# Performance work log

Hardware: AMD Instinct MI355X
Metric: run time of the kernel (lower is better)

Reference implementation:

```python
import jax, jax.numpy as jnp
import numpy as np

# Explicit-duration HSMM forward DP in log space.
# Recursion (all quantities in log space):
#   entry[t, j] = pi[j]                                   if t == 0
#               = logsumexp_i alpha[t-1, i] + A[i, j]      otherwise
#   alpha[t, j] = logsumexp_{d=1..min(Dmax, t+1)}
#                   entry[t-d+1, j] + D[j, d] + sum_{u=t-d+1..t} log_B[u, j]
#   loglik      = logsumexp_j alpha[T-1, j]

NEG = -1.0e30  # finite -inf sentinel (autodiff-safe)
B, T, S, DMAX = 64, 2048, 128, 128


def setup_inputs() -> dict:
    key = jax.random.key(0)
    k1, k2, k3, k4 = jax.random.split(key, 4)
    # emission log-likelihoods per (batch, time, state); need not normalize over states
    log_B = jax.random.normal(k1, (B, T, S), dtype=jnp.float32)
    # normalized log-prob buffers, matching the module's buffer constraints
    pi_logits = jax.nn.log_softmax(jax.random.normal(k2, (S,), dtype=jnp.float32))
    A_raw = jax.random.normal(k3, (S, S), dtype=jnp.float32)
    # SEMI transition constraint: no self-transitions (diagonal ~ -inf), rows normalized
    A_logits = jax.nn.log_softmax(
        jnp.where(jnp.eye(S, dtype=bool), -1.0e9, A_raw), axis=1)
    D_logits = jax.nn.log_softmax(
        jax.random.normal(k4, (S, DMAX), dtype=jnp.float32), axis=1)
    return {"log_B": log_B, "pi_logits": pi_logits,
            "A_logits": A_logits, "D_logits": D_logits}


def _hsmm_forward_loglik(log_B, pi_logits, A_logits, D_logits):
    Bn, Tn, Sn = log_B.shape
    Dm = D_logits.shape[1]
    lb = jnp.transpose(log_B, (1, 0, 2))                         # (T, B, S)
    # cum[k] = sum_{u < k} log_B[u]; front-padded with Dm zero rows (masked anyway)
    cum = jnp.concatenate(
        [jnp.zeros((1, Bn, Sn), lb.dtype), jnp.cumsum(lb, axis=0)], axis=0)
    cum_pad = jnp.concatenate(
        [jnp.zeros((Dm, Bn, Sn), lb.dtype), cum], axis=0)        # (T+Dm+1, B, S)
    logD = D_logits.T[:, None, :]                                # (Dm, 1, S)
    dur = jnp.arange(1, Dm + 1)[:, None, None]                   # (Dm, 1, 1)

    def step(carry, t):
        entry_buf, alpha_prev = carry                            # (Dm,B,S), (B,S)
        # transition into state j after a segment ended at t-1
        trans = jax.nn.logsumexp(
            alpha_prev[:, :, None] + A_logits[None, :, :], axis=1)  # (B, S)
        entry_t = jnp.where(t == 0, pi_logits[None, :], trans)
        # entry_buf[d-1] = entry[t-d+1]
        entry_buf = jnp.roll(entry_buf, 1, axis=0).at[0].set(entry_t)
        # segment emission sums: seg[d-1] = cum[t+1] - cum[t+1-d]
        win = jax.lax.dynamic_slice_in_dim(cum_pad, t + 1, Dm, axis=0)
        end = jax.lax.dynamic_slice_in_dim(cum_pad, t + Dm + 1, 1, axis=0)
        seg = end - jnp.flip(win, axis=0)                        # (Dm, B, S)
        scores = entry_buf + logD + seg
        scores = jnp.where(dur <= t + 1, scores, NEG)            # mask d > t+1
        alpha_t = jax.nn.logsumexp(scores, axis=0)               # (B, S)
        return (entry_buf, alpha_t), None

    init = (jnp.full((Dm, Bn, Sn), NEG, lb.dtype),
            jnp.full((Bn, Sn), NEG, lb.dtype))
    (_, alpha_last), _ = jax.lax.scan(step, init, jnp.arange(Tn))
    return jax.nn.logsumexp(alpha_last, axis=1)                  # (B,)


def reference(log_B, pi_logits, A_logits, D_logits):
    return _hsmm_forward_loglik(log_B, pi_logits, A_logits, D_logits)
```

## Files before the change

### kernel.cpp

```cpp
#include <hip/hip_runtime.h>

#define TT 2048
#define SS 128
#define DMAXX 128
#define NBATCH 64

typedef float f2 __attribute__((ext_vector_type(2)));

__device__ __forceinline__ float fexp2(float x){ return __builtin_amdgcn_exp2f(x); }
__device__ __forceinline__ float flog2(float x){ return __builtin_amdgcn_logf(x); }
__device__ __forceinline__ float frcp (float x){ return __builtin_amdgcn_rcpf(x); }
__device__ __forceinline__ f2 pkfma(f2 a, f2 b, f2 c){ return __builtin_elementwise_fma(a, b, c); }

template<int CTRL>
__device__ __forceinline__ float dppf(float x) {
    int i = __float_as_int(x);
    return __int_as_float(__builtin_amdgcn_update_dpp(i, i, CTRL, 0xF, 0xF, false));
}
#define DPP_XOR1   0xB1
#define DPP_XOR2   0x4E
#define DPP_SHUP1  0x90
#define DPP_ROR4   0x124
#define DPP_ROR8   0x128
#define DPP_BC15   0x142
#define DPP_BC31   0x143

constexpr float LOG2E = 1.4426950408889634f;
constexpr float LN2   = 0.6931471805599453f;

struct State {
    f2    rp[16];
    f2    eAp[16];
    f2    eDp[32];
    float eD0;
    float pf[4];
    const float* pfp;
    float C2;
    float e_pi;
};

struct Ctx {
    const float4* up0; const float4* up1;
    const f2*     wmp;
    float* uaw0; float* uaw1;
    float* wmwp;
    bool q0, l63;
};

template<int PHI>
__device__ __forceinline__ void hsmm_step(State& st, const Ctx& c, int tb)
{
    constexpr int  rho   = 31 - PHI;
    constexpr int  pb    = (PHI + 1) & 1;
    constexpr int  wb    = PHI & 1;
    constexpr bool DO_WM = ((PHI & 7) == 6);
    constexpr bool DO_RN = ((PHI & 7) == 7);
    const int t = tb + PHI;

    const float4* up = pb ? c.up1 : c.up0;
    float4 v[8];
#pragma unroll
    for (int k = 0; k < 8; ++k) v[k] = up[k];

    float xB = st.pf[PHI & 3];
    if (t + 4 < TT) st.pf[PHI & 3] = st.pfp[0];
    st.pfp += SS;
    float g = fexp2(xB * LOG2E);
    if constexpr (DO_RN) {
        f2 wv = *c.wmp;
        float m = fmaxf(wv.x, wv.y);
        m = fmaxf(m, dppf<DPP_XOR1>(m));
        m = fmaxf(m, dppf<DPP_XOR2>(m));
        st.C2 += flog2(m);
        g *= frcp(m);
    }

    float rold;
    if constexpr (rho & 1) rold = st.rp[rho >> 1].y; else rold = st.rp[rho >> 1].x;
    float car  = dppf<DPP_SHUP1>(rold);
    float insg = (c.q0 ? 0.f : car) * g;
    f2 gg = {g, g};
#pragma unroll
    for (int m2 = 0; m2 < 16; ++m2) st.rp[m2] = st.rp[m2] * gg;
    if constexpr (rho & 1) st.rp[rho >> 1].y = insg;
    else                   st.rp[rho >> 1].x = insg;

    f2 q0a = {0.f, 0.f}, q1a = {0.f, 0.f}, q2a = {0.f, 0.f}, q3a = {0.f, 0.f};
#pragma unroll
    for (int m2 = 0; m2 < 16; m2 += 4) {
        q0a = pkfma(st.rp[m2],     st.eDp[(2 * m2 + PHI + 1) & 31], q0a);
        q1a = pkfma(st.rp[m2 + 1], st.eDp[(2 * m2 + PHI + 3) & 31], q1a);
        q2a = pkfma(st.rp[m2 + 2], st.eDp[(2 * m2 + PHI + 5) & 31], q2a);
        q3a = pkfma(st.rp[m2 + 3], st.eDp[(2 * m2 + PHI + 7) & 31], q3a);
    }
    f2 qs = (q0a + q1a) + (q2a + q3a);
    float ds = qs.x + qs.y;
    ds += dppf<DPP_XOR1>(ds);
    ds += dppf<DPP_XOR2>(ds);

    f2 a0, a1, a2, a3;
    {
        f2 u;
        u = (f2){v[0].x, v[0].y}; a0 = u * st.eAp[0];
        u = (f2){v[0].z, v[0].w}; a1 = u * st.eAp[1];
        u = (f2){v[1].x, v[1].y}; a2 = u * st.eAp[2];
        u = (f2){v[1].z, v[1].w}; a3 = u * st.eAp[3];
#pragma unroll
        for (int kk = 2; kk < 8; kk += 2) {
            u = (f2){v[kk].x,     v[kk].y};     a0 = pkfma(u, st.eAp[2 * kk],     a0);
            u = (f2){v[kk].z,     v[kk].w};     a1 = pkfma(u, st.eAp[2 * kk + 1], a1);
            u = (f2){v[kk + 1].x, v[kk + 1].y}; a2 = pkfma(u, st.eAp[2 * kk + 2], a2);
            u = (f2){v[kk + 1].z, v[kk + 1].w}; a3 = pkfma(u, st.eAp[2 * kk + 3], a3);
        }
    }
    f2 asum = (a0 + a1) + (a2 + a3);
    float tp = asum.x + asum.y;
    tp += dppf<DPP_XOR1>(tp);
    tp += dppf<DPP_XOR2>(tp);
    if constexpr (PHI == 0) { if (tb == 0) tp = st.e_pi; }

    float tpg = tp * g;
    float U = fmaf(tpg, st.eD0, ds);
    if (c.q0) {
        if constexpr (rho & 1) st.rp[rho >> 1].y = tpg;
        else                   st.rp[rho >> 1].x = tpg;
    }
    if (c.q0) *(wb ? c.uaw1 : c.uaw0) = U;

    if constexpr (DO_WM) {
        float wm = U;
        wm = fmaxf(wm, dppf<DPP_ROR4>(wm));
        wm = fmaxf(wm, dppf<DPP_ROR8>(wm));
        wm = fmaxf(wm, dppf<DPP_BC15>(wm));
        wm = fmaxf(wm, dppf<DPP_BC31>(wm));
        if (c.l63) *c.wmwp = wm;
    }

    asm volatile("s_waitcnt lgkmcnt(0)\n\ts_barrier" ::: "memory");
}

__launch_bounds__(512, 2)
__global__ void hsmm_fwd_kernel(const float* __restrict__ logB,
                                const float* __restrict__ pi,
                                const float* __restrict__ A,
                                const float* __restrict__ D,
                                float* __restrict__ out)
{
    const int b   = blockIdx.x;
    const int tid = threadIdx.x;
    const int l   = tid & 63;
    const int w   = tid >> 6;
    const int j   = tid >> 2;
    const int q   = tid & 3;

    __shared__ __align__(16) float ua[2][4 * 36];
    __shared__ __align__(16) float wmaxf[8];

    State st;
#pragma unroll
    for (int k = 0; k < 16; ++k) {
        st.eAp[k].x = fexp2(A[(q * 32 + 2 * k)     * SS + j] * LOG2E);
        st.eAp[k].y = fexp2(A[(q * 32 + 2 * k + 1) * SS + j] * LOG2E);
    }
    {
        float eD[32];
#pragma unroll
        for (int k = 0; k < 32; ++k)
            eD[k] = fexp2(D[j * DMAXX + q * 32 + k] * LOG2E);
#pragma unroll
        for (int wdx = 0; wdx < 32; ++wdx) {
            st.eDp[wdx].x = eD[wdx];
            st.eDp[wdx].y = eD[(wdx + 1) & 31];
        }
    }
#pragma unroll
    for (int k = 0; k < 16; ++k) st.rp[k] = (f2){0.f, 0.f};
    st.eD0  = fexp2(D[j * DMAXX] * LOG2E);
    st.C2   = 0.f;
    st.e_pi = fexp2(pi[j] * LOG2E);

    const float* __restrict__ lb = logB + ((size_t)b * TT) * SS + j;
#pragma unroll
    for (int k = 0; k < 4; ++k) st.pf[k] = lb[(size_t)k * SS];
    st.pfp = lb + (size_t)4 * SS;

    Ctx c;
    c.up0  = (const float4*)&ua[0][q * 36];
    c.up1  = (const float4*)&ua[1][q * 36];
    c.wmp  = (const f2*)&wmaxf[2 * q];
    c.q0   = (q == 0);
    c.l63  = (l == 63);
    c.uaw0 = &ua[0][(j >> 5) * 36 + (j & 31)];
    c.uaw1 = &ua[1][(j >> 5) * 36 + (j & 31)];
    c.wmwp = &wmaxf[w];

    for (int tb = 0; tb < TT; tb += 32) {
        hsmm_step< 0>(st, c, tb); hsmm_step< 1>(st, c, tb);
        hsmm_step< 2>(st, c, tb); hsmm_step< 3>(st, c, tb);
        hsmm_step< 4>(st, c, tb); hsmm_step< 5>(st, c, tb);
        hsmm_step< 6>(st, c, tb); hsmm_step< 7>(st, c, tb);
        hsmm_step< 8>(st, c, tb); hsmm_step< 9>(st, c, tb);
        hsmm_step<10>(st, c, tb); hsmm_step<11>(st, c, tb);
        hsmm_step<12>(st, c, tb); hsmm_step<13>(st, c, tb);
        hsmm_step<14>(st, c, tb); hsmm_step<15>(st, c, tb);
        hsmm_step<16>(st, c, tb); hsmm_step<17>(st, c, tb);
        hsmm_step<18>(st, c, tb); hsmm_step<19>(st, c, tb);
        hsmm_step<20>(st, c, tb); hsmm_step<21>(st, c, tb);
        hsmm_step<22>(st, c, tb); hsmm_step<23>(st, c, tb);
        hsmm_step<24>(st, c, tb); hsmm_step<25>(st, c, tb);
        hsmm_step<26>(st, c, tb); hsmm_step<27>(st, c, tb);
        hsmm_step<28>(st, c, tb); hsmm_step<29>(st, c, tb);
        hsmm_step<30>(st, c, tb); hsmm_step<31>(st, c, tb);
    }

    if (tid == 0) {
        float s = 0.f;
        for (int i = 0; i < SS; ++i) s += ua[1][(i >> 5) * 36 + (i & 31)];
        out[b] = (st.C2 + flog2(s)) * LN2;
    }
}

extern "C" void kernel_launch(void* const* d_in, const int* in_sizes, int n_in,
                              void* d_out, int out_size, void* d_ws, size_t ws_size,
                              hipStream_t stream) {
    const float* logB = (const float*)d_in[0];
    const float* pi   = (const float*)d_in[1];
    const float* A    = (const float*)d_in[2];
    const float* D    = (const float*)d_in[3];
    float* out        = (float*)d_out;
    hipLaunchKernelGGL(hsmm_fwd_kernel, dim3(NBATCH), dim3(512), 0, stream,
                       logB, pi, A, D, out);
}
```

Before: 961.1 us.

## Defer ring rescaling with cumulative scale factor and precompute duration sum

Replaces the per-step multiply of all 32 ring-buffer entries by g with a running cumulative scale G. New entries are stored divided by G, and the whole ring is rebased only once every 32 steps. The duration dot product for the next step is computed at the end of the current step, after the barrier-gated work, so it sits off the critical path between the shared-memory read and the store. This cuts the VALU work per step and shortens the serial chain. The cost is an extra reciprocal per step and possible range loss, since G can grow or shrink across 32 steps between rebases.

```diff
diff --git a/kernel.cpp b/kernel.cpp
--- a/kernel.cpp
+++ b/kernel.cpp
@@ -37,6 +37,8 @@
     const float* pfp;
     float C2;
     float e_pi;
+    float G;
+    float dsP;
 };
 
 struct Ctx {
@@ -50,11 +52,13 @@
 template<int PHI>
 __device__ __forceinline__ void hsmm_step(State& st, const Ctx& c, int tb)
 {
-    constexpr int  rho   = 31 - PHI;
-    constexpr int  pb    = (PHI + 1) & 1;
-    constexpr int  wb    = PHI & 1;
-    constexpr bool DO_WM = ((PHI & 7) == 6);
-    constexpr bool DO_RN = ((PHI & 7) == 7);
+    constexpr int  rho    = 31 - PHI;
+    constexpr int  rhoN   = 31 - ((PHI + 1) & 31);
+    constexpr int  pb     = (PHI + 1) & 1;
+    constexpr int  wb     = PHI & 1;
+    constexpr bool DO_WM  = ((PHI & 7) == 6);
+    constexpr bool DO_RN  = ((PHI & 7) == 7);
+    constexpr bool REBASE = (PHI == 31);
     const int t = tb + PHI;
 
     const float4* up = pb ? c.up1 : c.up0;
@@ -74,29 +78,9 @@
         st.C2 += flog2(m);
         g *= frcp(m);
     }
-
-    float rold;
-    if constexpr (rho & 1) rold = st.rp[rho >> 1].y; else rold = st.rp[rho >> 1].x;
-    float car  = dppf<DPP_SHUP1>(rold);
-    float insg = (c.q0 ? 0.f : car) * g;
-    f2 gg = {g, g};
-#pragma unroll
-    for (int m2 = 0; m2 < 16; ++m2) st.rp[m2] = st.rp[m2] * gg;
-    if constexpr (rho & 1) st.rp[rho >> 1].y = insg;
-    else                   st.rp[rho >> 1].x = insg;
-
-    f2 q0a = {0.f, 0.f}, q1a = {0.f, 0.f}, q2a = {0.f, 0.f}, q3a = {0.f, 0.f};
-#pragma unroll
-    for (int m2 = 0; m2 < 16; m2 += 4) {
-        q0a = pkfma(st.rp[m2],     st.eDp[(2 * m2 + PHI + 1) & 31], q0a);
-        q1a = pkfma(st.rp[m2 + 1], st.eDp[(2 * m2 + PHI + 3) & 31], q1a);
-        q2a = pkfma(st.rp[m2 + 2], st.eDp[(2 * m2 + PHI + 5) & 31], q2a);
-        q3a = pkfma(st.rp[m2 + 3], st.eDp[(2 * m2 + PHI + 7) & 31], q3a);
-    }
-    f2 qs = (q0a + q1a) + (q2a + q3a);
-    float ds = qs.x + qs.y;
-    ds += dppf<DPP_XOR1>(ds);
-    ds += dppf<DPP_XOR2>(ds);
+    float rG = frcp(st.G);
+    float Gn = st.G * g;
+    st.G = Gn;
 
     f2 a0, a1, a2, a3;
     {
@@ -119,13 +103,13 @@
     tp += dppf<DPP_XOR2>(tp);
     if constexpr (PHI == 0) { if (tb == 0) tp = st.e_pi; }
 
-    float tpg = tp * g;
-    float U = fmaf(tpg, st.eD0, ds);
+    float U = fmaf(tp * g, st.eD0, st.dsP * Gn);
     if (c.q0) {
-        if constexpr (rho & 1) st.rp[rho >> 1].y = tpg;
-        else                   st.rp[rho >> 1].x = tpg;
-    }
-    if (c.q0) *(wb ? c.uaw1 : c.uaw0) = U;
+        float fr = tp * rG;
+        if constexpr (rho & 1) st.rp[rho >> 1].y = fr;
+        else                   st.rp[rho >> 1].x = fr;
+        *(wb ? c.uaw1 : c.uaw0) = U;
+    }
 
     if constexpr (DO_WM) {
         float wm = U;
@@ -135,6 +119,34 @@
         wm = fmaxf(wm, dppf<DPP_BC31>(wm));
         if (c.l63) *c.wmwp = wm;
     }
+
+    if constexpr (REBASE) {
+        f2 GG = {Gn, Gn};
+#pragma unroll
+        for (int m2 = 0; m2 < 16; ++m2) st.rp[m2] = st.rp[m2] * GG;
+        st.G = 1.f;
+    }
+
+    float rold;
+    if constexpr (rhoN & 1) rold = st.rp[rhoN >> 1].y; else rold = st.rp[rhoN >> 1].x;
+    float car = dppf<DPP_SHUP1>(rold);
+    float ins = c.q0 ? 0.f : car;
+    if constexpr (rhoN & 1) st.rp[rhoN >> 1].y = ins;
+    else                    st.rp[rhoN >> 1].x = ins;
+
+    f2 q0a = {0.f, 0.f}, q1a = {0.f, 0.f}, q2a = {0.f, 0.f}, q3a = {0.f, 0.f};
+#pragma unroll
+    for (int m2 = 0; m2 < 16; m2 += 4) {
+        q0a = pkfma(st.rp[m2],     st.eDp[(2 * m2 + PHI + 2) & 31], q0a);
+        q1a = pkfma(st.rp[m2 + 1], st.eDp[(2 * m2 + PHI + 4) & 31], q1a);
+        q2a = pkfma(st.rp[m2 + 2], st.eDp[(2 * m2 + PHI + 6) & 31], q2a);
+        q3a = pkfma(st.rp[m2 + 3], st.eDp[(2 * m2 + PHI + 8) & 31], q3a);
+    }
+    f2 qs = (q0a + q1a) + (q2a + q3a);
+    float ds = qs.x + qs.y;
+    ds += dppf<DPP_XOR1>(ds);
+    ds += dppf<DPP_XOR2>(ds);
+    st.dsP = ds;
 
     asm volatile("s_waitcnt lgkmcnt(0)\n\ts_barrier" ::: "memory");
 }
@@ -178,6 +190,8 @@
     st.eD0  = fexp2(D[j * DMAXX] * LOG2E);
     st.C2   = 0.f;
     st.e_pi = fexp2(pi[j] * LOG2E);
+    st.G    = 1.f;
+    st.dsP  = 0.f;
 
     const float* __restrict__ lb = logB + ((size_t)b * TT) * SS + j;
 #pragma unroll
```

Result: faster. 830.8 us (-13.6%).
